# Kernel tuning notes

Measured on AMD Instinct MI355X. Metric: run time of the kernel, lower is better.

The kernel has to match this reference:

```python
import jax, jax.numpy as jnp
import numpy as np

B, L, D = 4, 2048, 1024
E, K, H = 8, 2, 4096
EPS = 1e-5


def setup_inputs() -> dict:
    key = jax.random.key(0)
    ks = jax.random.split(key, 6)
    x = jax.random.normal(ks[0], (B, L, D), jnp.float32)
    gate_w = jax.random.normal(ks[1], (E, D), jnp.float32) * 0.02
    W1 = jax.random.normal(ks[2], (E, D, H), jnp.float32) * 0.02
    b1 = jnp.zeros((E, H), jnp.float32)
    W2 = jax.random.normal(ks[3], (E, H, D), jnp.float32) * 0.02
    b2 = jnp.zeros((E, D), jnp.float32)
    gamma = jnp.ones((D,), jnp.float32)
    beta = jnp.zeros((D,), jnp.float32)
    return {"x": x, "gamma": gamma, "beta": beta, "gate_w": gate_w,
            "W1": W1, "b1": b1, "W2": W2, "b2": b2}


def reference(x, gamma, beta, gate_w, W1, b1, W2, b2):
    # LayerNorm (biased variance, eps=1e-5, matches torch.nn.LayerNorm)
    mu = jnp.mean(x, axis=-1, keepdims=True)
    var = jnp.mean((x - mu) ** 2, axis=-1, keepdims=True)
    xn = (x - mu) / jnp.sqrt(var + EPS) * gamma + beta
    xf = xn.reshape(-1, D)  # (T, D), T = B*L
    T = xf.shape[0]

    # gating: top-k logits -> softmax -> scatter into dense gates (T, E)
    logits = xf @ gate_w.T  # (T, E)
    top_v, top_i = jax.lax.top_k(logits, K)
    top_g = jax.nn.softmax(top_v, axis=-1)
    gates = jnp.zeros_like(logits).at[jnp.arange(T)[:, None], top_i].set(top_g)

    # experts: dense-equivalent of masked gather/FFN/scatter-add combine.
    # Non-selected experts contribute with gate weight 0 -> identical math.
    h = jax.nn.gelu(jnp.einsum('td,edh->teh', xf, W1) + b1, approximate=False)
    y = jnp.einsum('teh,ehd->ted', h, W2) + b2  # (T, E, D)
    out = jnp.einsum('te,ted->td', gates, y).reshape(B, L, D) + x

    # load-balance loss: MSE(mean gate per expert, uniform)
    load = jnp.mean(gates, axis=0)
    bal_loss = jnp.mean((load - 1.0 / E) ** 2)
    return out, bal_loss
```

## Files before the change

kernel.cpp:

```cpp
#include <hip/hip_runtime.h>
#include <hip/hip_bf16.h>

#define T_TOK 8192
#define DD 1024
#define EE 8
#define HH 4096
#define NA (2 * T_TOK)
#define NBLK (NA / 256)

typedef __bf16 bf16_t;
typedef __bf16 bf16x8 __attribute__((ext_vector_type(8)));
typedef __bf16 bf16x4 __attribute__((ext_vector_type(4)));
typedef float f32x4 __attribute__((ext_vector_type(4)));

#define GLDS(g, l) __builtin_amdgcn_global_load_lds( \
    (const __attribute__((address_space(1))) void*)(g), \
    (__attribute__((address_space(3))) void*)(l), 16, 0, 0)

__device__ __forceinline__ float gelu_fast(float v) {
    float u = v * (0.79788456080286536f + 0.035677408136300125f * v * v);
    float a = 2.8853900817779268f * u;
    a = fminf(fmaxf(a, -87.0f), 87.0f);
    float t = __builtin_amdgcn_exp2f(a);
    return v * t * __builtin_amdgcn_rcpf(t + 1.0f);
}

__global__ __launch_bounds__(256) void ln_gate_kernel(
    const float* __restrict__ x, const float* __restrict__ gamma,
    const float* __restrict__ beta, const float* __restrict__ gate_w,
    bf16_t* __restrict__ xn, int* __restrict__ tokexp, float* __restrict__ tokgate)
{
    const int t = blockIdx.x;
    const int tid = threadIdx.x;
    const int lane = tid & 63, wave = tid >> 6;
    __shared__ float wred[4];
    __shared__ float stats[2];
    __shared__ float lred[32];
    __shared__ float logitsS[8];

    float4 v = ((const float4*)(x + (size_t)t * DD))[tid];
    float s = v.x + v.y + v.z + v.w;
#pragma unroll
    for (int o = 32; o > 0; o >>= 1) s += __shfl_down(s, o, 64);
    if (lane == 0) wred[wave] = s;
    __syncthreads();
    if (tid == 0) stats[0] = (wred[0] + wred[1] + wred[2] + wred[3]) * (1.0f / DD);
    __syncthreads();
    const float mu = stats[0];
    float d0 = v.x - mu, d1 = v.y - mu, d2 = v.z - mu, d3 = v.w - mu;
    float q = d0*d0 + d1*d1 + d2*d2 + d3*d3;
#pragma unroll
    for (int o = 32; o > 0; o >>= 1) q += __shfl_down(q, o, 64);
    __syncthreads();
    if (lane == 0) wred[wave] = q;
    __syncthreads();
    if (tid == 0) stats[1] = rsqrtf((wred[0]+wred[1]+wred[2]+wred[3]) * (1.0f / DD) + 1e-5f);
    __syncthreads();
    const float rstd = stats[1];
    float4 g4 = ((const float4*)gamma)[tid];
    float4 b4 = ((const float4*)beta)[tid];
    float n0 = d0 * rstd * g4.x + b4.x;
    float n1 = d1 * rstd * g4.y + b4.y;
    float n2 = d2 * rstd * g4.z + b4.z;
    float n3 = d3 * rstd * g4.w + b4.w;
    bf16x4 pk = { (bf16_t)n0, (bf16_t)n1, (bf16_t)n2, (bf16_t)n3 };
    ((bf16x4*)(xn + (size_t)t * DD))[tid] = pk;

    float part[8];
#pragma unroll
    for (int e = 0; e < 8; ++e) {
        float4 gw = ((const float4*)(gate_w + (size_t)e * DD))[tid];
        part[e] = n0 * gw.x + n1 * gw.y + n2 * gw.z + n3 * gw.w;
    }
#pragma unroll
    for (int e = 0; e < 8; ++e) {
        float p = part[e];
#pragma unroll
        for (int o = 32; o > 0; o >>= 1) p += __shfl_down(p, o, 64);
        if (lane == 0) lred[wave * 8 + e] = p;
    }
    __syncthreads();
    if (tid < 8) logitsS[tid] = lred[tid] + lred[8 + tid] + lred[16 + tid] + lred[24 + tid];
    __syncthreads();
    if (tid == 0) {
        float best = -1e30f; int e0 = 0;
        for (int e = 0; e < 8; ++e) { float le = logitsS[e]; if (le > best) { best = le; e0 = e; } }
        float best2 = -1e30f; int e1 = (e0 == 0) ? 1 : 0;
        for (int e = 0; e < 8; ++e) if (e != e0) { float le = logitsS[e]; if (le > best2) { best2 = le; e1 = e; } }
        float z = expf(best2 - best);
        float g0 = 1.0f / (1.0f + z);
        float g1 = z * g0;
        tokexp[2*t] = e0; tokexp[2*t+1] = e1;
        tokgate[2*t] = g0; tokgate[2*t+1] = g1;
    }
}

__global__ __launch_bounds__(256) void hist_kernel(
    const int* __restrict__ tokexp, const float* __restrict__ tokgate,
    int* __restrict__ blockcnt, float* __restrict__ blockgsum)
{
    __shared__ int hcnt[EE];
    __shared__ float hg[EE];
    const int b = blockIdx.x, tid = threadIdx.x;
    if (tid < EE) { hcnt[tid] = 0; hg[tid] = 0.f; }
    __syncthreads();
    int idx = b * 256 + tid;
    int e = tokexp[idx];
    atomicAdd(&hcnt[e], 1);
    atomicAdd(&hg[e], tokgate[idx]);
    __syncthreads();
    if (tid < EE) {
        blockcnt[b * EE + tid] = hcnt[tid];
        blockgsum[b * EE + tid] = hg[tid];
    }
}

__global__ __launch_bounds__(64) void offs_bal_kernel(
    const int* __restrict__ blockcnt, const float* __restrict__ blockgsum,
    int* __restrict__ cnt, int* __restrict__ offs, int* __restrict__ basep,
    float* __restrict__ bal_out)
{
    __shared__ int cntS[EE];
    const int tid = threadIdx.x;
    if (tid < EE) {
        int run = 0;
        for (int b = 0; b < NBLK; ++b) {
            basep[b * EE + tid] = run;
            run += blockcnt[b * EE + tid];
        }
        cnt[tid] = run;
        cntS[tid] = run;
    }
    __syncthreads();
    __shared__ int offsS[EE];
    if (tid == 0) {
        int run = 0; 
        for (int e = 0; e < EE; ++e) { offsS[e] = run; offs[e] = run; run += cntS[e]; }
        float bal = 0.f;
        for (int e = 0; e < EE; ++e) {
            float g = 0.f;
            for (int b = 0; b < NBLK; ++b) g += blockgsum[b * EE + e];
            float l = g * (1.0f / T_TOK) - (1.0f / EE);
            bal += l * l;
        }
        bal_out[0] = bal * (1.0f / EE);
    }
    __syncthreads();
    if (tid < EE) {
        for (int b = 0; b < NBLK; ++b) basep[b * EE + tid] += offsS[tid];
    }
}

__global__ __launch_bounds__(256) void scatter_kernel(
    const int* __restrict__ tokexp, const float* __restrict__ tokgate,
    const int* __restrict__ basep,
    int* __restrict__ tok, float* __restrict__ gatev, int* __restrict__ a_of_t)
{
    __shared__ int hcnt[EE];
    const int b = blockIdx.x, tid = threadIdx.x;
    if (tid < EE) hcnt[tid] = 0;
    __syncthreads();
    int idx = b * 256 + tid;
    int e = tokexp[idx];
    int r = atomicAdd(&hcnt[e], 1);
    int a = basep[b * EE + e] + r;
    tok[a] = idx >> 1;
    gatev[a] = tokgate[idx];
    a_of_t[idx] = a;
}

__global__ __launch_bounds__(256) void convT_kernel(
    const float* __restrict__ in, bf16_t* __restrict__ out, int R, int C)
{
    __shared__ float tile[64][65];
    int e = blockIdx.z;
    int c0 = blockIdx.x * 64, r0 = blockIdx.y * 64;
    int tx = threadIdx.x & 63, ty = threadIdx.x >> 6;
    const float* src = in + ((size_t)e * R + r0) * C + c0;
#pragma unroll
    for (int i = 0; i < 16; ++i) {
        int r = ty + i * 4;
        tile[r][tx] = src[(size_t)r * C + tx];
    }
    __syncthreads();
    bf16_t* dst = out + ((size_t)e * C + c0) * R + r0;
#pragma unroll
    for (int i = 0; i < 16; ++i) {
        int cc = ty + i * 4;
        dst[(size_t)cc * R + tx] = (bf16_t)tile[tx][cc];
    }
}


__global__ __launch_bounds__(512, 2) void ffn1_kernel(
    const bf16_t* __restrict__ xn, const bf16_t* __restrict__ w1t,
    const float* __restrict__ b1, const int* __restrict__ tok,
    const int* __restrict__ cnt, const int* __restrict__ offs,
    bf16_t* __restrict__ h1)
{
    const int e = blockIdx.z;
    const int c = cnt[e];
    const int m0 = blockIdx.y * 256;
    if (m0 >= c) return;
    const int n0 = blockIdx.x * 256;
    const int off = offs[e];

    __shared__ __align__(16) bf16_t As[2][256 * 64];
    __shared__ __align__(16) bf16_t Bs[2][256 * 64];

    const int tid = threadIdx.x;
    const int rloc = tid >> 3;
    const int qx8 = ((tid & 7) ^ (rloc & 7)) * 8;

    int mA0 = m0 + rloc;        if (mA0 >= c) mA0 = c - 1;
    int mA1 = m0 + 64 + rloc;   if (mA1 >= c) mA1 = c - 1;
    int mA2 = m0 + 128 + rloc;  if (mA2 >= c) mA2 = c - 1;
    int mA3 = m0 + 192 + rloc;  if (mA3 >= c) mA3 = c - 1;
    const bf16_t* pa0 = xn + (size_t)tok[off + mA0] * DD + qx8;
    const bf16_t* pa1 = xn + (size_t)tok[off + mA1] * DD + qx8;
    const bf16_t* pa2 = xn + (size_t)tok[off + mA2] * DD + qx8;
    const bf16_t* pa3 = xn + (size_t)tok[off + mA3] * DD + qx8;
    const bf16_t* pb0 = w1t + ((size_t)e * HH + n0 + rloc) * DD + qx8;
    const bf16_t* pb1 = pb0 + (size_t)64 * DD;
    const bf16_t* pb2 = pb0 + (size_t)128 * DD;
    const bf16_t* pb3 = pb0 + (size_t)192 * DD;

    const int lane = tid & 63, wave = tid >> 6;
    const int wm = wave >> 2, wn = wave & 3;
    const int l15 = lane & 15, lq = lane >> 4;
    const int rx = l15 & 7;
    const int rowA = (wm * 128 + l15) * 64;
    const int rowB = (wn * 64 + l15) * 64;
    const int cs0 = ((0 + lq) ^ rx) * 8;
    const int cs1 = ((4 + lq) ^ rx) * 8;

    f32x4 acc[8][4] = {};

    auto stage = [&](int buf) {
        bf16_t* la = &As[buf][tid * 8];
        bf16_t* lb = &Bs[buf][tid * 8];
        GLDS(pa0, la);          GLDS(pa1, la + 4096);
        GLDS(pa2, la + 8192);   GLDS(pa3, la + 12288);
        GLDS(pb0, lb);          GLDS(pb1, lb + 4096);
        GLDS(pb2, lb + 8192);   GLDS(pb3, lb + 12288);
        pa0 += 64; pa1 += 64; pa2 += 64; pa3 += 64;
        pb0 += 64; pb1 += 64; pb2 += 64; pb3 += 64;
    };

    stage(0);
    const int NT = DD / 64;
    for (int t = 0; t < NT; ++t) {
        const int cur = t & 1;
        if (t + 1 < NT) {
            stage(cur ^ 1);
            asm volatile("s_waitcnt vmcnt(8)" ::: "memory");
        } else {
            asm volatile("s_waitcnt vmcnt(0)" ::: "memory");
        }
        __builtin_amdgcn_s_barrier();
        const bf16_t* Ab = &As[cur][0];
        const bf16_t* Bb = &Bs[cur][0];
#pragma unroll
        for (int kk = 0; kk < 2; ++kk) {
            const int cs = kk ? cs1 : cs0;
            bf16x8 wf[4], xf[8];
#pragma unroll
            for (int nf = 0; nf < 4; ++nf)
                wf[nf] = *(const bf16x8*)(Bb + rowB + nf * 1024 + cs);
#pragma unroll
            for (int tf = 0; tf < 8; ++tf)
                xf[tf] = *(const bf16x8*)(Ab + rowA + tf * 1024 + cs);
#pragma unroll
            for (int tf = 0; tf < 8; ++tf)
#pragma unroll
                for (int nf = 0; nf < 4; ++nf)
                    acc[tf][nf] = __builtin_amdgcn_mfma_f32_16x16x32_bf16(
                        wf[nf], xf[tf], acc[tf][nf], 0, 0, 0);
        }
        asm volatile("s_waitcnt lgkmcnt(0)" ::: "memory");
        __builtin_amdgcn_s_barrier();
    }

    const float* b1e = b1 + (size_t)e * HH;
#pragma unroll
    for (int tf = 0; tf < 8; ++tf) {
        int m = m0 + wm * 128 + tf * 16 + l15;
        if (m < c) {
            bf16_t* hrow = h1 + (size_t)(off + m) * HH;
#pragma unroll
            for (int nf = 0; nf < 4; ++nf) {
                int n = n0 + wn * 64 + nf * 16 + lq * 4;
                float4 bb = *(const float4*)(b1e + n);
                f32x4 a = acc[tf][nf];
                bf16x4 pk;
                pk[0] = (bf16_t)gelu_fast(a[0] + bb.x);
                pk[1] = (bf16_t)gelu_fast(a[1] + bb.y);
                pk[2] = (bf16_t)gelu_fast(a[2] + bb.z);
                pk[3] = (bf16_t)gelu_fast(a[3] + bb.w);
                *(bf16x4*)(hrow + n) = pk;
            }
        }
    }
}

__global__ __launch_bounds__(512, 2) void ffn2_kernel(
    const bf16_t* __restrict__ h1, const bf16_t* __restrict__ w2t,
    const float* __restrict__ b2, const float* __restrict__ gatev,
    const int* __restrict__ cnt, const int* __restrict__ offs,
    bf16_t* __restrict__ yv)
{
    const int e = blockIdx.z;
    const int c = cnt[e];
    const int m0 = blockIdx.y * 256;
    if (m0 >= c) return;
    const int n0 = blockIdx.x * 256;
    const int off = offs[e];

    __shared__ __align__(16) bf16_t As[2][256 * 64];
    __shared__ __align__(16) bf16_t Bs[2][256 * 64];

    const int tid = threadIdx.x;
    const int rloc = tid >> 3;
    const int qx8 = ((tid & 7) ^ (rloc & 7)) * 8;

    int mA0 = m0 + rloc;        if (mA0 >= c) mA0 = c - 1;
    int mA1 = m0 + 64 + rloc;   if (mA1 >= c) mA1 = c - 1;
    int mA2 = m0 + 128 + rloc;  if (mA2 >= c) mA2 = c - 1;
    int mA3 = m0 + 192 + rloc;  if (mA3 >= c) mA3 = c - 1;
    const bf16_t* pa0 = h1 + (size_t)(off + mA0) * HH + qx8;
    const bf16_t* pa1 = h1 + (size_t)(off + mA1) * HH + qx8;
    const bf16_t* pa2 = h1 + (size_t)(off + mA2) * HH + qx8;
    const bf16_t* pa3 = h1 + (size_t)(off + mA3) * HH + qx8;
    const bf16_t* pb0 = w2t + ((size_t)e * DD + n0 + rloc) * HH + qx8;
    const bf16_t* pb1 = pb0 + (size_t)64 * HH;
    const bf16_t* pb2 = pb0 + (size_t)128 * HH;
    const bf16_t* pb3 = pb0 + (size_t)192 * HH;

    const int lane = tid & 63, wave = tid >> 6;
    const int wm = wave >> 2, wn = wave & 3;
    const int l15 = lane & 15, lq = lane >> 4;
    const int rx = l15 & 7;
    const int rowA = (wm * 128 + l15) * 64;
    const int rowB = (wn * 64 + l15) * 64;
    const int cs0 = ((0 + lq) ^ rx) * 8;
    const int cs1 = ((4 + lq) ^ rx) * 8;

    f32x4 acc[8][4] = {};

    auto stage = [&](int buf) {
        bf16_t* la = &As[buf][tid * 8];
        bf16_t* lb = &Bs[buf][tid * 8];
        GLDS(pa0, la);          GLDS(pa1, la + 4096);
        GLDS(pa2, la + 8192);   GLDS(pa3, la + 12288);
        GLDS(pb0, lb);          GLDS(pb1, lb + 4096);
        GLDS(pb2, lb + 8192);   GLDS(pb3, lb + 12288);
        pa0 += 64; pa1 += 64; pa2 += 64; pa3 += 64;
        pb0 += 64; pb1 += 64; pb2 += 64; pb3 += 64;
    };

    stage(0);
    const int NT = HH / 64;
    for (int t = 0; t < NT; ++t) {
        const int cur = t & 1;
        if (t + 1 < NT) {
            stage(cur ^ 1);
            asm volatile("s_waitcnt vmcnt(8)" ::: "memory");
        } else {
            asm volatile("s_waitcnt vmcnt(0)" ::: "memory");
        }
        __builtin_amdgcn_s_barrier();
        const bf16_t* Ab = &As[cur][0];
        const bf16_t* Bb = &Bs[cur][0];
#pragma unroll
        for (int kk = 0; kk < 2; ++kk) {
            const int cs = kk ? cs1 : cs0;
            bf16x8 wf[4], xf[8];
#pragma unroll
            for (int nf = 0; nf < 4; ++nf)
                wf[nf] = *(const bf16x8*)(Bb + rowB + nf * 1024 + cs);
#pragma unroll
            for (int tf = 0; tf < 8; ++tf)
                xf[tf] = *(const bf16x8*)(Ab + rowA + tf * 1024 + cs);
#pragma unroll
            for (int tf = 0; tf < 8; ++tf)
#pragma unroll
                for (int nf = 0; nf < 4; ++nf)
                    acc[tf][nf] = __builtin_amdgcn_mfma_f32_16x16x32_bf16(
                        wf[nf], xf[tf], acc[tf][nf], 0, 0, 0);
        }
        asm volatile("s_waitcnt lgkmcnt(0)" ::: "memory");
        __builtin_amdgcn_s_barrier();
    }

    const float* b2e = b2 + (size_t)e * DD;
#pragma unroll
    for (int tf = 0; tf < 8; ++tf) {
        int m = m0 + wm * 128 + tf * 16 + l15;
        if (m < c) {
            float g = gatev[off + m];
            bf16_t* yrow = yv + (size_t)(off + m) * DD;
#pragma unroll
            for (int nf = 0; nf < 4; ++nf) {
                int n = n0 + wn * 64 + nf * 16 + lq * 4;
                float4 bb = *(const float4*)(b2e + n);
                f32x4 a = acc[tf][nf];
                bf16x4 pk;
                pk[0] = (bf16_t)((a[0] + bb.x) * g);
                pk[1] = (bf16_t)((a[1] + bb.y) * g);
                pk[2] = (bf16_t)((a[2] + bb.z) * g);
                pk[3] = (bf16_t)((a[3] + bb.w) * g);
                *(bf16x4*)(yrow + n) = pk;
            }
        }
    }
}

__global__ __launch_bounds__(256) void combine_kernel(
    const float* __restrict__ x, const bf16_t* __restrict__ yv,
    const int* __restrict__ a_of_t, float* __restrict__ outp)
{
    int t = blockIdx.x;
    int tid = threadIdx.x;
    int a0 = a_of_t[2*t], a1 = a_of_t[2*t+1];
    float4 xv = ((const float4*)(x + (size_t)t * DD))[tid];
    bf16x4 y0 = ((const bf16x4*)(yv + (size_t)a0 * DD))[tid];
    bf16x4 y1 = ((const bf16x4*)(yv + (size_t)a1 * DD))[tid];
    float4 o;
    o.x = xv.x + (float)y0[0] + (float)y1[0];
    o.y = xv.y + (float)y0[1] + (float)y1[1];
    o.z = xv.z + (float)y0[2] + (float)y1[2];
    o.w = xv.w + (float)y0[3] + (float)y1[3];
    ((float4*)(outp + (size_t)t * DD))[tid] = o;
}

extern "C" void kernel_launch(void* const* d_in, const int* in_sizes, int n_in,
                              void* d_out, int out_size, void* d_ws, size_t ws_size,
                              hipStream_t stream)
{
    const float* x      = (const float*)d_in[0];
    const float* gamma  = (const float*)d_in[1];
    const float* beta   = (const float*)d_in[2];
    const float* gate_w = (const float*)d_in[3];
    const float* W1     = (const float*)d_in[4];
    const float* b1     = (const float*)d_in[5];
    const float* W2     = (const float*)d_in[6];
    const float* b2     = (const float*)d_in[7];
    float* outp = (float*)d_out;
    float* bal_out = outp + (size_t)T_TOK * DD;

    char* ws = (char*)d_ws;
    size_t off = 0;
    auto alloc = [&](size_t bytes) {
        char* p = ws + off;
        off += (bytes + 255) & ~(size_t)255;
        return p;
    };
    bf16_t* xn   = (bf16_t*)alloc((size_t)T_TOK * DD * 2);
    bf16_t* w1t  = (bf16_t*)alloc((size_t)EE * HH * DD * 2);
    bf16_t* w2t  = (bf16_t*)alloc((size_t)EE * DD * HH * 2);
    bf16_t* h1   = (bf16_t*)alloc((size_t)NA * HH * 2);
    bf16_t* yv   = (bf16_t*)alloc((size_t)NA * DD * 2);
    int*   tok     = (int*)alloc(NA * 4);
    float* gatev   = (float*)alloc(NA * 4);
    int*   a_of_t  = (int*)alloc(NA * 4);
    int*   tokexp  = (int*)alloc(NA * 4);
    float* tokgate = (float*)alloc(NA * 4);
    int*   blockcnt  = (int*)alloc(NBLK * EE * 4);
    float* blockgsum = (float*)alloc(NBLK * EE * 4);
    int*   basep     = (int*)alloc(NBLK * EE * 4);
    int*   cnt  = (int*)alloc(EE * 4);
    int*   offs = (int*)alloc(EE * 4);

    convT_kernel<<<dim3(HH/64, DD/64, EE), 256, 0, stream>>>(W1, w1t, DD, HH);
    convT_kernel<<<dim3(DD/64, HH/64, EE), 256, 0, stream>>>(W2, w2t, HH, DD);
    ln_gate_kernel<<<T_TOK, 256, 0, stream>>>(x, gamma, beta, gate_w, xn, tokexp, tokgate);
    hist_kernel<<<NBLK, 256, 0, stream>>>(tokexp, tokgate, blockcnt, blockgsum);
    offs_bal_kernel<<<1, 64, 0, stream>>>(blockcnt, blockgsum, cnt, offs, basep, bal_out);
    scatter_kernel<<<NBLK, 256, 0, stream>>>(tokexp, tokgate, basep, tok, gatev, a_of_t);
    ffn1_kernel<<<dim3(HH/256, 32, EE), 512, 0, stream>>>(xn, w1t, b1, tok, cnt, offs, h1);
    ffn2_kernel<<<dim3(DD/256, 32, EE), 512, 0, stream>>>(h1, w2t, b2, gatev, cnt, offs, yv);
    combine_kernel<<<T_TOK, 256, 0, stream>>>(x, yv, a_of_t, outp);
}
```

Measured before the change: 868.5 us.

## Rewrite expert GEMM mainloop as four-phase pipelined schedule with inline-asm LDS reads

Replaces the simple double-buffered mainloop in both expert GEMMs with a shared templated mainloop. Each K tile is split into four sub-phases that interleave global-to-LDS loads, explicit ds_read_b128 fragment loads and 16-MFMA blocks, using s_setprio and sched_barrier. The wave-to-output-column mapping changes, so the epilogues are updated to match. The aim is to hide LDS read and global load latency behind MFMA work and cut register pressure, at the cost of more barriers and fragile hand-placed waitcnt counts.

```diff
diff --git a/kernel.cpp b/kernel.cpp
--- a/kernel.cpp
+++ b/kernel.cpp
@@ -12,10 +12,18 @@
 typedef __bf16 bf16x8 __attribute__((ext_vector_type(8)));
 typedef __bf16 bf16x4 __attribute__((ext_vector_type(4)));
 typedef float f32x4 __attribute__((ext_vector_type(4)));
+typedef int   i32x4 __attribute__((ext_vector_type(4)));
+
+union frag_u { i32x4 i; bf16x8 b; };
 
 #define GLDS(g, l) __builtin_amdgcn_global_load_lds( \
     (const __attribute__((address_space(1))) void*)(g), \
     (__attribute__((address_space(3))) void*)(l), 16, 0, 0)
+
+#define DSR(d, a)      asm volatile("ds_read_b128 %0, %1"           : "=v"(d) : "v"(a))
+#define DSRO(d, a, O)  asm volatile("ds_read_b128 %0, %1 offset:" O : "=v"(d) : "v"(a))
+
+#define VMW(N) asm volatile("s_waitcnt vmcnt(" #N ")" ::: "memory")
 
 __device__ __forceinline__ float gelu_fast(float v) {
     float u = v * (0.79788456080286536f + 0.035677408136300125f * v * v);
@@ -192,6 +200,126 @@
 }
 
 
+#define MM(tf, nf) \
+    acc[tf][nf] = __builtin_amdgcn_mfma_f32_16x16x32_bf16(bB[(nf)&1][0].b, aA[(tf)&3][0].b, acc[tf][nf], 0,0,0); \
+    acc[tf][nf] = __builtin_amdgcn_mfma_f32_16x16x32_bf16(bB[(nf)&1][1].b, aA[(tf)&3][1].b, acc[tf][nf], 0,0,0);
+
+#define MFMA16(mq, nq) \
+    MM((mq)*4+0, (nq)*2+0) MM((mq)*4+0, (nq)*2+1) \
+    MM((mq)*4+1, (nq)*2+0) MM((mq)*4+1, (nq)*2+1) \
+    MM((mq)*4+2, (nq)*2+0) MM((mq)*4+2, (nq)*2+1) \
+    MM((mq)*4+3, (nq)*2+0) MM((mq)*4+3, (nq)*2+1)
+
+#define LOAD_A(mq_) do { \
+    uint32_t a0_ = abase0 + rb + (mq_)*8192u; \
+    uint32_t a1_ = abase1 + rb + (mq_)*8192u; \
+    DSR (aA[0][0].i, a0_); DSRO(aA[1][0].i, a0_, "2048"); \
+    DSRO(aA[2][0].i, a0_, "4096"); DSRO(aA[3][0].i, a0_, "6144"); \
+    DSR (aA[0][1].i, a1_); DSRO(aA[1][1].i, a1_, "2048"); \
+    DSRO(aA[2][1].i, a1_, "4096"); DSRO(aA[3][1].i, a1_, "6144"); \
+} while (0)
+
+#define LOAD_B(nq_) do { \
+    uint32_t b0_ = bbase0 + rb + (nq_)*32768u; \
+    uint32_t b1_ = bbase1 + rb + (nq_)*32768u; \
+    DSR (bB[0][0].i, b0_); DSRO(bB[1][0].i, b0_, "2048"); \
+    DSR (bB[0][1].i, b1_); DSRO(bB[1][1].i, b1_, "2048"); \
+} while (0)
+
+#define PHASE_MID() do { \
+    __builtin_amdgcn_s_barrier(); \
+    asm volatile("s_waitcnt lgkmcnt(0)" ::: "memory"); \
+    __builtin_amdgcn_sched_barrier(0); \
+    __builtin_amdgcn_s_setprio(1); \
+} while (0)
+
+#define PHASE_END() do { \
+    __builtin_amdgcn_s_setprio(0); \
+    __builtin_amdgcn_s_barrier(); \
+} while (0)
+
+template<int NT>
+__device__ __forceinline__ void mfma_mainloop(
+    const bf16_t* pa0, const bf16_t* pa1, const bf16_t* pa2, const bf16_t* pa3,
+    const bf16_t* pb0, const bf16_t* pb1, const bf16_t* pb2, const bf16_t* pb3,
+    bf16_t* S, f32x4 (&acc)[8][4])
+{
+    const int tid = threadIdx.x;
+    const int lane = tid & 63, wave = tid >> 6;
+    const int wm = wave >> 2, wn = wave & 3;
+    const int l15 = lane & 15, lq = lane >> 4, rx = l15 & 7;
+    const uint32_t csb0 = (uint32_t)((lq ^ rx) * 16);
+    const uint32_t csb1 = (uint32_t)(((4 + lq) ^ rx) * 16);
+    const uint32_t sbase = (uint32_t)(size_t)(__attribute__((address_space(3))) bf16_t*)S;
+    const uint32_t abase0 = sbase + (uint32_t)wm*32768u + (uint32_t)l15*128u + csb0;
+    const uint32_t abase1 = sbase + (uint32_t)wm*32768u + (uint32_t)l15*128u + csb1;
+    const uint32_t bbase0 = sbase + 16384u + (uint32_t)wn*4096u + (uint32_t)l15*128u + csb0;
+    const uint32_t bbase1 = sbase + 16384u + (uint32_t)wn*4096u + (uint32_t)l15*128u + csb1;
+
+    frag_u aA[4][2];
+    frag_u bB[2][2];
+
+    {
+        bf16_t* wb = S;
+        GLDS(pa0, wb +     0 + tid*8); pa0 += 64;
+        GLDS(pa2, wb + 16384 + tid*8); pa2 += 64;
+        GLDS(pb0, wb +  8192 + tid*8); pb0 += 64;
+        GLDS(pb1, wb + 12288 + tid*8); pb1 += 64;
+        GLDS(pa1, wb +  4096 + tid*8); pa1 += 64;
+        GLDS(pa3, wb + 20480 + tid*8); pa3 += 64;
+        GLDS(pb2, wb + 24576 + tid*8); pb2 += 64;
+        GLDS(pb3, wb + 28672 + tid*8); pb3 += 64;
+    }
+    VMW(4);
+    __builtin_amdgcn_s_barrier();
+
+    for (int kt = 0; kt < NT; ++kt) {
+        const uint32_t rb = (uint32_t)(kt & 1) * 65536u;
+        bf16_t* wb = S + (size_t)(((kt + 1) & 1)) * 32768;
+        const bool more = (kt + 1 < NT);
+
+        LOAD_A(0); LOAD_B(0);
+        if (more) {
+            GLDS(pa0, wb +     0 + tid*8); pa0 += 64;
+            GLDS(pa2, wb + 16384 + tid*8); pa2 += 64;
+            VMW(4);
+        } else VMW(2);
+        PHASE_MID();
+        MFMA16(0, 0)
+        PHASE_END();
+
+        LOAD_A(1);
+        if (more) {
+            GLDS(pb0, wb +  8192 + tid*8); pb0 += 64;
+            GLDS(pb1, wb + 12288 + tid*8); pb1 += 64;
+            VMW(4);
+        } else VMW(0);
+        PHASE_MID();
+        MFMA16(1, 0)
+        PHASE_END();
+
+        LOAD_B(1);
+        if (more) {
+            GLDS(pa1, wb +  4096 + tid*8); pa1 += 64;
+            GLDS(pa3, wb + 20480 + tid*8); pa3 += 64;
+            VMW(4);
+        }
+        PHASE_MID();
+        MFMA16(1, 1)
+        PHASE_END();
+
+        LOAD_A(0);
+        if (more) {
+            GLDS(pb2, wb + 24576 + tid*8); pb2 += 64;
+            GLDS(pb3, wb + 28672 + tid*8); pb3 += 64;
+            VMW(4);
+        }
+        PHASE_MID();
+        MFMA16(0, 1)
+        PHASE_END();
+    }
+}
+
 __global__ __launch_bounds__(512, 2) void ffn1_kernel(
     const bf16_t* __restrict__ xn, const bf16_t* __restrict__ w1t,
     const float* __restrict__ b1, const int* __restrict__ tok,
@@ -205,8 +333,7 @@
     const int n0 = blockIdx.x * 256;
     const int off = offs[e];
 
-    __shared__ __align__(16) bf16_t As[2][256 * 64];
-    __shared__ __align__(16) bf16_t Bs[2][256 * 64];
+    __shared__ __align__(16) bf16_t S[2 * 4 * 8192];
 
     const int tid = threadIdx.x;
     const int rloc = tid >> 3;
@@ -225,61 +352,12 @@
     const bf16_t* pb2 = pb0 + (size_t)128 * DD;
     const bf16_t* pb3 = pb0 + (size_t)192 * DD;
 
+    f32x4 acc[8][4] = {};
+    mfma_mainloop<DD / 64>(pa0, pa1, pa2, pa3, pb0, pb1, pb2, pb3, S, acc);
+
     const int lane = tid & 63, wave = tid >> 6;
     const int wm = wave >> 2, wn = wave & 3;
     const int l15 = lane & 15, lq = lane >> 4;
-    const int rx = l15 & 7;
-    const int rowA = (wm * 128 + l15) * 64;
-    const int rowB = (wn * 64 + l15) * 64;
-    const int cs0 = ((0 + lq) ^ rx) * 8;
-    const int cs1 = ((4 + lq) ^ rx) * 8;
-
-    f32x4 acc[8][4] = {};
-
-    auto stage = [&](int buf) {
-        bf16_t* la = &As[buf][tid * 8];
-        bf16_t* lb = &Bs[buf][tid * 8];
-        GLDS(pa0, la);          GLDS(pa1, la + 4096);
-        GLDS(pa2, la + 8192);   GLDS(pa3, la + 12288);
-        GLDS(pb0, lb);          GLDS(pb1, lb + 4096);
-        GLDS(pb2, lb + 8192);   GLDS(pb3, lb + 12288);
-        pa0 += 64; pa1 += 64; pa2 += 64; pa3 += 64;
-        pb0 += 64; pb1 += 64; pb2 += 64; pb3 += 64;
-    };
-
-    stage(0);
-    const int NT = DD / 64;
-    for (int t = 0; t < NT; ++t) {
-        const int cur = t & 1;
-        if (t + 1 < NT) {
-            stage(cur ^ 1);
-            asm volatile("s_waitcnt vmcnt(8)" ::: "memory");
-        } else {
-            asm volatile("s_waitcnt vmcnt(0)" ::: "memory");
-        }
-        __builtin_amdgcn_s_barrier();
-        const bf16_t* Ab = &As[cur][0];
-        const bf16_t* Bb = &Bs[cur][0];
-#pragma unroll
-        for (int kk = 0; kk < 2; ++kk) {
-            const int cs = kk ? cs1 : cs0;
-            bf16x8 wf[4], xf[8];
-#pragma unroll
-            for (int nf = 0; nf < 4; ++nf)
-                wf[nf] = *(const bf16x8*)(Bb + rowB + nf * 1024 + cs);
-#pragma unroll
-            for (int tf = 0; tf < 8; ++tf)
-                xf[tf] = *(const bf16x8*)(Ab + rowA + tf * 1024 + cs);
-#pragma unroll
-            for (int tf = 0; tf < 8; ++tf)
-#pragma unroll
-                for (int nf = 0; nf < 4; ++nf)
-                    acc[tf][nf] = __builtin_amdgcn_mfma_f32_16x16x32_bf16(
-                        wf[nf], xf[tf], acc[tf][nf], 0, 0, 0);
-        }
-        asm volatile("s_waitcnt lgkmcnt(0)" ::: "memory");
-        __builtin_amdgcn_s_barrier();
-    }
 
     const float* b1e = b1 + (size_t)e * HH;
 #pragma unroll
@@ -289,7 +367,7 @@
             bf16_t* hrow = h1 + (size_t)(off + m) * HH;
 #pragma unroll
             for (int nf = 0; nf < 4; ++nf) {
-                int n = n0 + wn * 64 + nf * 16 + lq * 4;
+                int n = n0 + (nf >> 1) * 128 + wn * 32 + (nf & 1) * 16 + lq * 4;
                 float4 bb = *(const float4*)(b1e + n);
                 f32x4 a = acc[tf][nf];
                 bf16x4 pk;
@@ -316,8 +394,7 @@
     const int n0 = blockIdx.x * 256;
     const int off = offs[e];
 
-    __shared__ __align__(16) bf16_t As[2][256 * 64];
-    __shared__ __align__(16) bf16_t Bs[2][256 * 64];
+    __shared__ __align__(16) bf16_t S[2 * 4 * 8192];
 
     const int tid = threadIdx.x;
     const int rloc = tid >> 3;
@@ -336,61 +413,12 @@
     const bf16_t* pb2 = pb0 + (size_t)128 * HH;
     const bf16_t* pb3 = pb0 + (size_t)192 * HH;
 
+    f32x4 acc[8][4] = {};
+    mfma_mainloop<HH / 64>(pa0, pa1, pa2, pa3, pb0, pb1, pb2, pb3, S, acc);
+
     const int lane = tid & 63, wave = tid >> 6;
     const int wm = wave >> 2, wn = wave & 3;
     const int l15 = lane & 15, lq = lane >> 4;
-    const int rx = l15 & 7;
-    const int rowA = (wm * 128 + l15) * 64;
-    const int rowB = (wn * 64 + l15) * 64;
-    const int cs0 = ((0 + lq) ^ rx) * 8;
-    const int cs1 = ((4 + lq) ^ rx) * 8;
-
-    f32x4 acc[8][4] = {};
-
-    auto stage = [&](int buf) {
-        bf16_t* la = &As[buf][tid * 8];
-        bf16_t* lb = &Bs[buf][tid * 8];
-        GLDS(pa0, la);          GLDS(pa1, la + 4096);
-        GLDS(pa2, la + 8192);   GLDS(pa3, la + 12288);
-        GLDS(pb0, lb);          GLDS(pb1, lb + 4096);
-        GLDS(pb2, lb + 8192);   GLDS(pb3, lb + 12288);
-        pa0 += 64; pa1 += 64; pa2 += 64; pa3 += 64;
-        pb0 += 64; pb1 += 64; pb2 += 64; pb3 += 64;
-    };
-
-    stage(0);
-    const int NT = HH / 64;
-    for (int t = 0; t < NT; ++t) {
-        const int cur = t & 1;
-        if (t + 1 < NT) {
-            stage(cur ^ 1);
-            asm volatile("s_waitcnt vmcnt(8)" ::: "memory");
-        } else {
-            asm volatile("s_waitcnt vmcnt(0)" ::: "memory");
-        }
-        __builtin_amdgcn_s_barrier();
-        const bf16_t* Ab = &As[cur][0];
-        const bf16_t* Bb = &Bs[cur][0];
-#pragma unroll
-        for (int kk = 0; kk < 2; ++kk) {
-            const int cs = kk ? cs1 : cs0;
-            bf16x8 wf[4], xf[8];
-#pragma unroll
-            for (int nf = 0; nf < 4; ++nf)
-                wf[nf] = *(const bf16x8*)(Bb + rowB + nf * 1024 + cs);
-#pragma unroll
-            for (int tf = 0; tf < 8; ++tf)
-                xf[tf] = *(const bf16x8*)(Ab + rowA + tf * 1024 + cs);
-#pragma unroll
-            for (int tf = 0; tf < 8; ++tf)
-#pragma unroll
-                for (int nf = 0; nf < 4; ++nf)
-                    acc[tf][nf] = __builtin_amdgcn_mfma_f32_16x16x32_bf16(
-                        wf[nf], xf[tf], acc[tf][nf], 0, 0, 0);
-        }
-        asm volatile("s_waitcnt lgkmcnt(0)" ::: "memory");
-        __builtin_amdgcn_s_barrier();
-    }
 
     const float* b2e = b2 + (size_t)e * DD;
 #pragma unroll
@@ -401,7 +429,7 @@
             bf16_t* yrow = yv + (size_t)(off + m) * DD;
 #pragma unroll
             for (int nf = 0; nf < 4; ++nf) {
-                int n = n0 + wn * 64 + nf * 16 + lq * 4;
+                int n = n0 + (nf >> 1) * 128 + wn * 32 + (nf & 1) * 16 + lq * 4;
                 float4 bb = *(const float4*)(b2e + n);
                 f32x4 a = acc[tf][nf];
                 bf16x4 pk;
```

New measurement: 781.7 us. 10.0% less time.
